# Kernel optimization log

Measured on AMD Instinct MI355X. Metric: run time of the kernel, lower is better.

The kernel has to match this reference:

```python
import jax, jax.numpy as jnp
import numpy as np

MARGIN = 1.0
EPS = 1e-12


def setup_inputs() -> dict:
    key = jax.random.key(0)
    k1, k2, k3 = jax.random.split(key, 3)
    inputs = jax.random.normal(k1, (8192, 128), dtype=jnp.float32)
    targets = jax.random.randint(k2, (8192,), 0, 64, dtype=jnp.int64)
    center = jax.random.normal(k3, (16, 128), dtype=jnp.float32)
    return {"inputs": inputs, "targets": targets, "center": center}


def reference(inputs, targets, center):
    n = inputs.shape[0]
    # pairwise Euclidean distances via ||a||^2 + ||b||^2 - 2 a.b  (matches addmm_ trick)
    sq = jnp.sum(inputs * inputs, axis=1)                      # [n]
    dist2 = sq[:, None] + sq[None, :] - 2.0 * (inputs @ inputs.T)
    dist = jnp.sqrt(jnp.clip(dist2, EPS))                      # [n, n]

    mask = targets[:, None] == targets[None, :]                # same-class mask [n, n]

    # batch-hard mining, fully vectorized (replaces per-row python loops)
    dist_ap = jnp.max(jnp.where(mask, dist, -jnp.inf), axis=1)  # hardest positive
    neg_min = jnp.min(jnp.where(mask, jnp.inf, dist), axis=1)   # hardest negative
    has_neg = jnp.any(~mask, axis=1)
    dist_an = jnp.where(has_neg, neg_min, dist_ap + MARGIN)

    # center augmentation: min over distances to L2-normalized prototypes
    cn = center / jnp.linalg.norm(center, axis=1, keepdims=True)       # [P, d]
    dc = jnp.sqrt(jnp.sum((inputs[:, None, :] - cn[None, :, :]) ** 2, axis=-1))  # [n, P]
    dc = jnp.clip(dc, EPS)
    dist_an = jnp.minimum(dist_an, jnp.min(dc, axis=1))

    # MarginRankingLoss with y=1: mean(relu(dist_ap - dist_an + margin))
    loss = jnp.mean(jnp.maximum(dist_ap - dist_an + MARGIN, 0.0))
    return loss
```

## Files before the change

kernel.cpp:

```cpp
#include <hip/hip_runtime.h>


#define N_ROWS 8192
#define DIM 128
#define KDIM 192
#define ROWB 384
#define NPROTO 16
#define MARGIN_F 1.0f
#define EPS_F 1e-12f
#define BIAS_F 32768.0f

typedef __attribute__((ext_vector_type(8))) short short8;
typedef __attribute__((ext_vector_type(4))) float float4v;
typedef __attribute__((ext_vector_type(4))) unsigned uint4v;

static __device__ __forceinline__ unsigned f2bf(float f) {
  unsigned u = __float_as_uint(f);
  u += 0x7fffu + ((u >> 16) & 1u);
  return u >> 16;
}

static __device__ __forceinline__ void gload_lds16(const void* g, void* l) {
  __builtin_amdgcn_global_load_lds(
      (const __attribute__((address_space(1))) unsigned*)g,
      (__attribute__((address_space(3))) unsigned*)l, 16, 0, 0);
}

__global__ void prep_kernel(const float* __restrict__ x,
                            const float* __restrict__ center,
                            const int* __restrict__ tgt,
                            char* __restrict__ xbf,
                            float* __restrict__ sq,
                            float* __restrict__ mindc,
                            float* __restrict__ out) {
  __shared__ float scn[NPROTO * DIM];
  int tid = threadIdx.x;
  if (blockIdx.x == 0 && tid == 0) out[0] = 0.0f;
  int rloc = tid >> 4, l = tid & 15;
  {
    float v[8];
    float ss = 0.f;
#pragma unroll
    for (int j = 0; j < 8; ++j) {
      v[j] = center[rloc * DIM + l * 8 + j];
      ss += v[j] * v[j];
    }
#pragma unroll
    for (int m = 1; m < 16; m <<= 1) ss += __shfl_xor(ss, m, 64);
    float inv = 1.0f / sqrtf(ss);
#pragma unroll
    for (int j = 0; j < 8; ++j) scn[rloc * DIM + l * 8 + j] = v[j] * inv;
  }
  __syncthreads();

  int row = blockIdx.x * 16 + rloc;
  float4 v0 = ((const float4*)x)[row * 32 + l * 2];
  float4 v1 = ((const float4*)x)[row * 32 + l * 2 + 1];
  float ss = v0.x * v0.x + v0.y * v0.y + v0.z * v0.z + v0.w * v0.w +
             v1.x * v1.x + v1.y * v1.y + v1.z * v1.z + v1.w * v1.w;
  float dots[NPROTO];
#pragma unroll
  for (int p = 0; p < NPROTO; ++p) {
    const float* c = &scn[p * DIM + l * 8];
    dots[p] = v0.x * c[0] + v0.y * c[1] + v0.z * c[2] + v0.w * c[3] +
              v1.x * c[4] + v1.y * c[5] + v1.z * c[6] + v1.w * c[7];
  }
#pragma unroll
  for (int m = 1; m < 16; m <<= 1) {
    ss += __shfl_xor(ss, m, 64);
#pragma unroll
    for (int p = 0; p < NPROTO; ++p) dots[p] += __shfl_xor(dots[p], m, 64);
  }
  uint4 pk;
  pk.x = f2bf(v0.x) | (f2bf(v0.y) << 16);
  pk.y = f2bf(v0.z) | (f2bf(v0.w) << 16);
  pk.z = f2bf(v1.x) | (f2bf(v1.y) << 16);
  pk.w = f2bf(v1.z) | (f2bf(v1.w) << 16);
  *(uint4*)(xbf + (size_t)row * ROWB + l * 16) = pk;
  int cls = tgt[row];
  if (l < 8) {
    unsigned wv = (cls & 1) ? 0xC3000000u : 0x0000C300u;
    uint4 oh;
    oh.x = ((cls >> 1) == (l * 4 + 0)) ? wv : 0u;
    oh.y = ((cls >> 1) == (l * 4 + 1)) ? wv : 0u;
    oh.z = ((cls >> 1) == (l * 4 + 2)) ? wv : 0u;
    oh.w = ((cls >> 1) == (l * 4 + 3)) ? wv : 0u;
    *(uint4*)(xbf + (size_t)row * ROWB + 256 + l * 16) = oh;
  }
  if (l == 0) {
    float mind2 = INFINITY;
#pragma unroll
    for (int p = 0; p < NPROTO; ++p)
      mind2 = fminf(mind2, ss + 1.0f - 2.0f * dots[p]);
    sq[row] = ss;
    mindc[row] = fmaxf(sqrtf(fmaxf(mind2, 0.0f)), EPS_F);
  }
}

__global__ __launch_bounds__(256, 2) void
pairdist_kernel(const char* __restrict__ xbf, const float* __restrict__ sq,
                float* __restrict__ pmax, float* __restrict__ pmin) {
  __shared__ __align__(16) char bl[2][24576];
  const int bid = blockIdx.x;
  const int rg = bid >> 4;
  const int strip = bid & 15;
  const int wave = threadIdx.x >> 6, lane = threadIdx.x & 63;
  const int q = lane >> 4, l16 = lane & 15;
  const int rowbase = rg * 256 + wave * 64;
  const int stripbase = strip * 512;

  const int slot = wave * 64 + lane;
  const char* const srcstrip = xbf + (size_t)stripbase * ROWB;
  int soff[6];
#pragma unroll
  for (int r = 0; r < 6; ++r) {
    int o = r * 4096 + slot * 16;
    int c = o / ROWB;
    soff[r] = c * ROWB + ((o - c * ROWB) ^ ((c & 7) << 4));
  }

  auto stage = [&](int s, char* buf) {
    const char* g = srcstrip + (size_t)s * 24576;
#pragma unroll
    for (int r = 0; r < 6; ++r)
      gload_lds16(g + soff[r], buf + r * 4096 + wave * 1024);
  };

  stage(0, bl[0]);

  short8 a[4][6];
#pragma unroll
  for (int rt = 0; rt < 4; ++rt) {
    const char* ar = xbf + (size_t)(rowbase + rt * 16 + l16) * ROWB + q * 16;
#pragma unroll
    for (int kc = 0; kc < 6; ++kc) a[rt][kc] = *(const short8*)(ar + kc * 64);
#pragma unroll
    for (int kc = 4; kc < 6; ++kc) {
      uint4v u = __builtin_bit_cast(uint4v, a[rt][kc]);
      u ^= 0x80008000u;
      a[rt][kc] = __builtin_bit_cast(short8, u);
    }
  }

  int roffb[6];
#pragma unroll
  for (int kc = 0; kc < 6; ++kc)
    roffb[kc] = (l16 * ROWB + kc * 64 + q * 16) ^ ((l16 & 7) << 4);

  float maxp[16], minn[16];
#pragma unroll
  for (int i = 0; i < 16; ++i) {
    maxp[i] = -INFINITY;
    minn[i] = INFINITY;
  }

#pragma unroll 1
  for (int s = 0; s < 8; ++s) {
    __syncthreads();
    if (s + 1 < 8) stage(s + 1, bl[(s + 1) & 1]);
    const char* cur = bl[s & 1];
    float sqs[4];
#pragma unroll
    for (int ss = 0; ss < 4; ++ss)
      sqs[ss] = sq[stripbase + s * 64 + ss * 16 + l16];
#pragma unroll
    for (int ss = 0; ss < 4; ++ss) {
      const char* bufp = cur + ss * 6144;
      short8 b[6];
#pragma unroll
      for (int kc = 0; kc < 6; ++kc)
        b[kc] = *(const short8*)(bufp + roffb[kc]);
      float4v acc[4];
#pragma unroll
      for (int rt = 0; rt < 4; ++rt) acc[rt] = (float4v){0.f, 0.f, 0.f, 0.f};
#pragma unroll
      for (int kc = 0; kc < 6; ++kc)
#pragma unroll
        for (int rt = 0; rt < 4; ++rt)
          acc[rt] = __builtin_amdgcn_mfma_f32_16x16x32_bf16(a[rt][kc], b[kc],
                                                            acc[rt], 0, 0, 0);
#pragma unroll
      for (int rt = 0; rt < 4; ++rt)
#pragma unroll
        for (int r = 0; r < 4; ++r) {
          float v = fmaf(-2.0f, acc[rt][r], sqs[ss]);
          int idx = rt * 4 + r;
          maxp[idx] = fmaxf(maxp[idx], v);
          minn[idx] = fminf(minn[idx], v);
        }
    }
  }

#pragma unroll
  for (int m = 1; m < 16; m <<= 1)
#pragma unroll
    for (int i = 0; i < 16; ++i) {
      maxp[i] = fmaxf(maxp[i], __shfl_xor(maxp[i], m, 64));
      minn[i] = fminf(minn[i], __shfl_xor(minn[i], m, 64));
    }
  if (l16 == 0) {
    float* pM = pmax + (size_t)strip * N_ROWS + rowbase + q * 4;
    float* pm = pmin + (size_t)strip * N_ROWS + rowbase + q * 4;
#pragma unroll
    for (int rt = 0; rt < 4; ++rt)
#pragma unroll
      for (int r = 0; r < 4; ++r) {
        pM[rt * 16 + r] = maxp[rt * 4 + r];
        pm[rt * 16 + r] = minn[rt * 4 + r];
      }
  }
}

__global__ void finalize_kernel(const float* __restrict__ pmax,
                                const float* __restrict__ pmin,
                                const float* __restrict__ sq,
                                const float* __restrict__ mindc,
                                float* __restrict__ out) {
  __shared__ float wsum[4];
  int i = blockIdx.x * 256 + threadIdx.x;
  float maxv = -INFINITY, minv = INFINITY;
#pragma unroll
  for (int s = 0; s < 16; ++s) {
    maxv = fmaxf(maxv, pmax[s * N_ROWS + i]);
    minv = fminf(minv, pmin[s * N_ROWS + i]);
  }
  float si = sq[i];
  float dap = sqrtf(fmaxf(si + (maxv - BIAS_F), EPS_F));
  float dan = (minv > 16384.0f) ? (dap + MARGIN_F)
                                : sqrtf(fmaxf(si + minv, EPS_F));
  dan = fminf(dan, mindc[i]);
  float c = fmaxf(dap - dan + MARGIN_F, 0.0f) * (1.0f / (float)N_ROWS);
#pragma unroll
  for (int m = 1; m < 64; m <<= 1) c += __shfl_xor(c, m, 64);
  int lane = threadIdx.x & 63, wv = threadIdx.x >> 6;
  if (lane == 0) wsum[wv] = c;
  __syncthreads();
  if (threadIdx.x == 0) atomicAdd(out, wsum[0] + wsum[1] + wsum[2] + wsum[3]);
}

extern "C" void kernel_launch(void* const* d_in, const int* in_sizes, int n_in,
                              void* d_out, int out_size, void* d_ws, size_t ws_size,
                              hipStream_t stream) {
  const float* inputs = (const float*)d_in[0];
  const int* targets = (const int*)d_in[1];
  const float* center = (const float*)d_in[2];
  char* ws = (char*)d_ws;
  char* xbf    = ws;
  float* sq    = (float*)(ws + 3145728);
  float* mindc = (float*)(ws + 3178496);
  float* pmax  = (float*)(ws + 3211264);
  float* pmin  = (float*)(ws + 3735552);
  float* out   = (float*)d_out;

  prep_kernel<<<512, 256, 0, stream>>>(inputs, center, targets, xbf, sq, mindc, out);
  pairdist_kernel<<<512, 256, 0, stream>>>(xbf, sq, pmax, pmin);
  finalize_kernel<<<32, 256, 0, stream>>>(pmax, pmin, sq, mindc, out);
}
```

Measured before the change: 92.99 us.

## Exploit distance-matrix symmetry by computing only upper-triangular 256x256 tiles

The pairwise kernel now launches 528 blocks covering only the upper-triangular 256x256 tiles (I<=J) instead of 512 blocks covering the full matrix. Each off-diagonal tile also derives column-wise max/min by reducing across lanes and waves through shared memory, then writes those as partials for the transposed rows. This roughly halves MFMA work, at the cost of an extra column reduction, shared-memory traffic, a second partial buffer layout (32 strips) and a longer finalize loop. Each block does half the columns it did before, so fixed per-block overhead weighs more.

```diff
diff --git a/kernel.cpp b/kernel.cpp
--- a/kernel.cpp
+++ b/kernel.cpp
@@ -6,6 +6,7 @@
 #define KDIM 192
 #define ROWB 384
 #define NPROTO 16
+#define NRG 32
 #define MARGIN_F 1.0f
 #define EPS_F 1e-12f
 #define BIAS_F 32768.0f
@@ -101,16 +102,17 @@
 pairdist_kernel(const char* __restrict__ xbf, const float* __restrict__ sq,
                 float* __restrict__ pmax, float* __restrict__ pmin) {
   __shared__ __align__(16) char bl[2][24576];
-  const int bid = blockIdx.x;
-  const int rg = bid >> 4;
-  const int strip = bid & 15;
+  __shared__ float cmaxw[4][256], cminw[4][256];
+  int t = blockIdx.x, I = 0;
+  while (t >= NRG - I) { t -= NRG - I; ++I; }
+  const int J = I + t;
   const int wave = threadIdx.x >> 6, lane = threadIdx.x & 63;
   const int q = lane >> 4, l16 = lane & 15;
-  const int rowbase = rg * 256 + wave * 64;
-  const int stripbase = strip * 512;
+  const int rowbase = I * 256 + wave * 64;
+  const int colbase = J * 256;
 
   const int slot = wave * 64 + lane;
-  const char* const srcstrip = xbf + (size_t)stripbase * ROWB;
+  const char* const srcstrip = xbf + (size_t)colbase * ROWB;
   int soff[6];
 #pragma unroll
   for (int r = 0; r < 6; ++r) {
@@ -141,6 +143,12 @@
       a[rt][kc] = __builtin_bit_cast(short8, u);
     }
   }
+  float sqr[16];
+#pragma unroll
+  for (int rt = 0; rt < 4; ++rt)
+#pragma unroll
+    for (int r = 0; r < 4; ++r)
+      sqr[rt * 4 + r] = sq[rowbase + rt * 16 + q * 4 + r];
 
   int roffb[6];
 #pragma unroll
@@ -155,14 +163,15 @@
   }
 
 #pragma unroll 1
-  for (int s = 0; s < 8; ++s) {
+  for (int s = 0; s < 4; ++s) {
     __syncthreads();
-    if (s + 1 < 8) stage(s + 1, bl[(s + 1) & 1]);
+    if (s + 1 < 4) stage(s + 1, bl[(s + 1) & 1]);
     const char* cur = bl[s & 1];
     float sqs[4];
 #pragma unroll
     for (int ss = 0; ss < 4; ++ss)
-      sqs[ss] = sq[stripbase + s * 64 + ss * 16 + l16];
+      sqs[ss] = sq[colbase + s * 64 + ss * 16 + l16];
+    float cmx[4], cmn[4];
 #pragma unroll
     for (int ss = 0; ss < 4; ++ss) {
       const char* bufp = cur + ss * 6144;
@@ -188,6 +197,32 @@
           maxp[idx] = fmaxf(maxp[idx], v);
           minn[idx] = fminf(minn[idx], v);
         }
+      if (I != J) {
+        float um = -INFINITY, un = INFINITY;
+#pragma unroll
+        for (int rt = 0; rt < 4; ++rt)
+#pragma unroll
+          for (int r = 0; r < 4; ++r) {
+            float u = fmaf(-2.0f, acc[rt][r], sqr[rt * 4 + r]);
+            um = fmaxf(um, u);
+            un = fminf(un, u);
+          }
+        cmx[ss] = um;
+        cmn[ss] = un;
+      }
+    }
+    if (I != J) {
+#pragma unroll
+      for (int ss = 0; ss < 4; ++ss) {
+        float a1 = fmaxf(cmx[ss], __shfl_xor(cmx[ss], 16, 64));
+        a1 = fmaxf(a1, __shfl_xor(a1, 32, 64));
+        float a2 = fminf(cmn[ss], __shfl_xor(cmn[ss], 16, 64));
+        a2 = fminf(a2, __shfl_xor(a2, 32, 64));
+        if (q == 0) {
+          cmaxw[wave][s * 64 + ss * 16 + l16] = a1;
+          cminw[wave][s * 64 + ss * 16 + l16] = a2;
+        }
+      }
     }
   }
 
@@ -199,8 +234,8 @@
       minn[i] = fminf(minn[i], __shfl_xor(minn[i], m, 64));
     }
   if (l16 == 0) {
-    float* pM = pmax + (size_t)strip * N_ROWS + rowbase + q * 4;
-    float* pm = pmin + (size_t)strip * N_ROWS + rowbase + q * 4;
+    float* pM = pmax + (size_t)J * N_ROWS + rowbase + q * 4;
+    float* pm = pmin + (size_t)J * N_ROWS + rowbase + q * 4;
 #pragma unroll
     for (int rt = 0; rt < 4; ++rt)
 #pragma unroll
@@ -208,6 +243,16 @@
         pM[rt * 16 + r] = maxp[rt * 4 + r];
         pm[rt * 16 + r] = minn[rt * 4 + r];
       }
+  }
+  if (I != J) {
+    __syncthreads();
+    int c = threadIdx.x;
+    float M = fmaxf(fmaxf(cmaxw[0][c], cmaxw[1][c]),
+                    fmaxf(cmaxw[2][c], cmaxw[3][c]));
+    float m = fminf(fminf(cminw[0][c], cminw[1][c]),
+                    fminf(cminw[2][c], cminw[3][c]));
+    pmax[(size_t)I * N_ROWS + colbase + c] = M;
+    pmin[(size_t)I * N_ROWS + colbase + c] = m;
   }
 }
 
@@ -220,7 +265,7 @@
   int i = blockIdx.x * 256 + threadIdx.x;
   float maxv = -INFINITY, minv = INFINITY;
 #pragma unroll
-  for (int s = 0; s < 16; ++s) {
+  for (int s = 0; s < NRG; ++s) {
     maxv = fmaxf(maxv, pmax[s * N_ROWS + i]);
     minv = fminf(minv, pmin[s * N_ROWS + i]);
   }
@@ -249,10 +294,10 @@
   float* sq    = (float*)(ws + 3145728);
   float* mindc = (float*)(ws + 3178496);
   float* pmax  = (float*)(ws + 3211264);
-  float* pmin  = (float*)(ws + 3735552);
+  float* pmin  = (float*)(ws + 4259840);
   float* out   = (float*)d_out;
 
   prep_kernel<<<512, 256, 0, stream>>>(inputs, center, targets, xbf, sq, mindc, out);
-  pairdist_kernel<<<512, 256, 0, stream>>>(xbf, sq, pmax, pmin);
+  pairdist_kernel<<<528, 256, 0, stream>>>(xbf, sq, pmax, pmin);
   finalize_kernel<<<32, 256, 0, stream>>>(pmax, pmin, sq, mindc, out);
 }
```

Result: slower. 110.7 us (+19.0%).

## Give each wave a private triple-buffered LDS pipeline to remove block barriers

Applied to the files above, without the earlier changes.

Each wave now streams its own 16-row chunks of the column strip into a private three-deep LDS ring, using explicit vmcnt waits instead of block-wide __syncthreads. MFMA sections are also wrapped in s_setprio to favour matrix issue. This removes barrier stalls between waves and deepens prefetch. In exchange, every wave loads the whole B strip itself, roughly quadrupling L2-to-LDS traffic and raising LDS use per block. The hand-written waitcnt counts also rely on how the compiler orders the per-chunk sq loads.

```diff
diff --git a/kernel.cpp b/kernel.cpp
--- a/kernel.cpp
+++ b/kernel.cpp
@@ -6,6 +6,8 @@
 #define KDIM 192
 #define ROWB 384
 #define NPROTO 16
+#define NSTRIP 16
+#define NCHUNK 32
 #define MARGIN_F 1.0f
 #define EPS_F 1e-12f
 #define BIAS_F 32768.0f
@@ -100,33 +102,29 @@
 __global__ __launch_bounds__(256, 2) void
 pairdist_kernel(const char* __restrict__ xbf, const float* __restrict__ sq,
                 float* __restrict__ pmax, float* __restrict__ pmin) {
-  __shared__ __align__(16) char bl[2][24576];
-  const int bid = blockIdx.x;
-  const int rg = bid >> 4;
-  const int strip = bid & 15;
+  __shared__ __align__(16) char bl[4][3 * 6144];
   const int wave = threadIdx.x >> 6, lane = threadIdx.x & 63;
   const int q = lane >> 4, l16 = lane & 15;
+  const int rg = blockIdx.x >> 4, strip = blockIdx.x & 15;
   const int rowbase = rg * 256 + wave * 64;
   const int stripbase = strip * 512;
-
-  const int slot = wave * 64 + lane;
-  const char* const srcstrip = xbf + (size_t)stripbase * ROWB;
+  char* const mybuf = bl[wave];
+
   int soff[6];
 #pragma unroll
   for (int r = 0; r < 6; ++r) {
-    int o = r * 4096 + slot * 16;
+    int o = r * 1024 + lane * 16;
     int c = o / ROWB;
     soff[r] = c * ROWB + ((o - c * ROWB) ^ ((c & 7) << 4));
   }
-
-  auto stage = [&](int s, char* buf) {
-    const char* g = srcstrip + (size_t)s * 24576;
-#pragma unroll
-    for (int r = 0; r < 6; ++r)
-      gload_lds16(g + soff[r], buf + r * 4096 + wave * 1024);
+  const char* const srcstrip = xbf + (size_t)stripbase * ROWB;
+
+  auto stage = [&](int ch, int bi) {
+    const char* g = srcstrip + (size_t)ch * 6144;
+    char* d = mybuf + bi * 6144;
+#pragma unroll
+    for (int r = 0; r < 6; ++r) gload_lds16(g + soff[r], d + r * 1024);
   };
-
-  stage(0, bl[0]);
 
   short8 a[4][6];
 #pragma unroll
@@ -141,6 +139,16 @@
       a[rt][kc] = __builtin_bit_cast(short8, u);
     }
   }
+#pragma unroll
+  for (int rt = 0; rt < 4; ++rt)
+#pragma unroll
+    for (int kc = 0; kc < 6; ++kc)
+      asm volatile("" : "+v"(a[rt][kc]));
+
+  asm volatile("s_waitcnt vmcnt(0)" ::: "memory");
+  stage(0, 0);
+  stage(1, 1);
+  stage(2, 2);
 
   int roffb[6];
 #pragma unroll
@@ -149,46 +157,45 @@
 
   float maxp[16], minn[16];
 #pragma unroll
-  for (int i = 0; i < 16; ++i) {
-    maxp[i] = -INFINITY;
-    minn[i] = INFINITY;
-  }
-
+  for (int i = 0; i < 16; ++i) { maxp[i] = -INFINITY; minn[i] = INFINITY; }
+
+  int bi = 0;
 #pragma unroll 1
-  for (int s = 0; s < 8; ++s) {
-    __syncthreads();
-    if (s + 1 < 8) stage(s + 1, bl[(s + 1) & 1]);
-    const char* cur = bl[s & 1];
-    float sqs[4];
-#pragma unroll
-    for (int ss = 0; ss < 4; ++ss)
-      sqs[ss] = sq[stripbase + s * 64 + ss * 16 + l16];
-#pragma unroll
-    for (int ss = 0; ss < 4; ++ss) {
-      const char* bufp = cur + ss * 6144;
-      short8 b[6];
-#pragma unroll
-      for (int kc = 0; kc < 6; ++kc)
-        b[kc] = *(const short8*)(bufp + roffb[kc]);
-      float4v acc[4];
-#pragma unroll
-      for (int rt = 0; rt < 4; ++rt) acc[rt] = (float4v){0.f, 0.f, 0.f, 0.f};
-#pragma unroll
-      for (int kc = 0; kc < 6; ++kc)
-#pragma unroll
-        for (int rt = 0; rt < 4; ++rt)
-          acc[rt] = __builtin_amdgcn_mfma_f32_16x16x32_bf16(a[rt][kc], b[kc],
-                                                            acc[rt], 0, 0, 0);
+  for (int c = 0; c < NCHUNK; ++c) {
+    if (c < NCHUNK - 2)
+      asm volatile("s_waitcnt vmcnt(12)" ::: "memory");
+    else if (c == NCHUNK - 2)
+      asm volatile("s_waitcnt vmcnt(6)" ::: "memory");
+    else
+      asm volatile("s_waitcnt vmcnt(0)" ::: "memory");
+    float sqc = sq[stripbase + c * 16 + l16];
+    const char* bufp = mybuf + bi * 6144;
+    short8 b[6];
+#pragma unroll
+    for (int kc = 0; kc < 6; ++kc) b[kc] = *(const short8*)(bufp + roffb[kc]);
+    asm volatile("s_waitcnt lgkmcnt(0)" ::: "memory");
+    if (c + 3 < NCHUNK) stage(c + 3, bi);
+    float4v acc[4];
+#pragma unroll
+    for (int rt = 0; rt < 4; ++rt) acc[rt] = (float4v){0.f, 0.f, 0.f, 0.f};
+    __builtin_amdgcn_s_setprio(1);
+#pragma unroll
+    for (int kc = 0; kc < 6; ++kc)
 #pragma unroll
       for (int rt = 0; rt < 4; ++rt)
-#pragma unroll
-        for (int r = 0; r < 4; ++r) {
-          float v = fmaf(-2.0f, acc[rt][r], sqs[ss]);
-          int idx = rt * 4 + r;
-          maxp[idx] = fmaxf(maxp[idx], v);
-          minn[idx] = fminf(minn[idx], v);
-        }
-    }
+        acc[rt] = __builtin_amdgcn_mfma_f32_16x16x32_bf16(a[rt][kc], b[kc],
+                                                          acc[rt], 0, 0, 0);
+    __builtin_amdgcn_s_setprio(0);
+#pragma unroll
+    for (int rt = 0; rt < 4; ++rt)
+#pragma unroll
+      for (int r = 0; r < 4; ++r) {
+        float v = fmaf(-2.0f, acc[rt][r], sqc);
+        int idx = rt * 4 + r;
+        maxp[idx] = fmaxf(maxp[idx], v);
+        minn[idx] = fminf(minn[idx], v);
+      }
+    if (++bi == 3) bi = 0;
   }
 
 #pragma unroll
@@ -220,7 +227,7 @@
   int i = blockIdx.x * 256 + threadIdx.x;
   float maxv = -INFINITY, minv = INFINITY;
 #pragma unroll
-  for (int s = 0; s < 16; ++s) {
+  for (int s = 0; s < NSTRIP; ++s) {
     maxv = fmaxf(maxv, pmax[s * N_ROWS + i]);
     minv = fminf(minv, pmin[s * N_ROWS + i]);
   }
```

Measured after the change: 98.28 us. +5.7%, slower.

## Switch pairwise-distance GEMM to 32x32x16 bf16 MFMA tiles

Applied to the files above, without the earlier changes.

Replaces the 16x16x32 MFMA tiling with 32x32x16 MFMA, so each wave computes two 32-row tiles against 32-column slices. Each B fragment read from LDS now feeds two MFMAs, and the register layout and final row/column reduction are rewritten to match the 32x32 output layout. Raises s_setprio around the MFMA loop and relaxes launch bounds to one block per SIMD pair, trading occupancy for more registers (32 max/min accumulators plus 16-wide accumulators).

```diff
diff --git a/kernel.cpp b/kernel.cpp
--- a/kernel.cpp
+++ b/kernel.cpp
@@ -6,12 +6,13 @@
 #define KDIM 192
 #define ROWB 384
 #define NPROTO 16
+#define NSTRIP 16
 #define MARGIN_F 1.0f
 #define EPS_F 1e-12f
 #define BIAS_F 32768.0f
 
 typedef __attribute__((ext_vector_type(8))) short short8;
-typedef __attribute__((ext_vector_type(4))) float float4v;
+typedef __attribute__((ext_vector_type(16))) float f32x16;
 typedef __attribute__((ext_vector_type(4))) unsigned uint4v;
 
 static __device__ __forceinline__ unsigned f2bf(float f) {
@@ -97,19 +98,17 @@
   }
 }
 
-__global__ __launch_bounds__(256, 2) void
+__global__ __launch_bounds__(256, 1) void
 pairdist_kernel(const char* __restrict__ xbf, const float* __restrict__ sq,
                 float* __restrict__ pmax, float* __restrict__ pmin) {
   __shared__ __align__(16) char bl[2][24576];
-  const int bid = blockIdx.x;
-  const int rg = bid >> 4;
-  const int strip = bid & 15;
   const int wave = threadIdx.x >> 6, lane = threadIdx.x & 63;
-  const int q = lane >> 4, l16 = lane & 15;
+  const int c31 = lane & 31, h = lane >> 5;
+  const int rg = blockIdx.x >> 4, strip = blockIdx.x & 15;
   const int rowbase = rg * 256 + wave * 64;
   const int stripbase = strip * 512;
 
-  const int slot = wave * 64 + lane;
+  const int slot = threadIdx.x;
   const char* const srcstrip = xbf + (size_t)stripbase * ROWB;
   int soff[6];
 #pragma unroll
@@ -128,85 +127,87 @@
 
   stage(0, bl[0]);
 
-  short8 a[4][6];
-#pragma unroll
-  for (int rt = 0; rt < 4; ++rt) {
-    const char* ar = xbf + (size_t)(rowbase + rt * 16 + l16) * ROWB + q * 16;
-#pragma unroll
-    for (int kc = 0; kc < 6; ++kc) a[rt][kc] = *(const short8*)(ar + kc * 64);
-#pragma unroll
-    for (int kc = 4; kc < 6; ++kc) {
-      uint4v u = __builtin_bit_cast(uint4v, a[rt][kc]);
+  short8 a[2][12];
+#pragma unroll
+  for (int t = 0; t < 2; ++t) {
+    const char* ar =
+        xbf + (size_t)(rowbase + t * 32 + c31) * ROWB + h * 16;
+#pragma unroll
+    for (int kc = 0; kc < 12; ++kc) a[t][kc] = *(const short8*)(ar + kc * 32);
+#pragma unroll
+    for (int kc = 8; kc < 12; ++kc) {
+      uint4v u = __builtin_bit_cast(uint4v, a[t][kc]);
       u ^= 0x80008000u;
-      a[rt][kc] = __builtin_bit_cast(short8, u);
-    }
-  }
-
-  int roffb[6];
-#pragma unroll
-  for (int kc = 0; kc < 6; ++kc)
-    roffb[kc] = (l16 * ROWB + kc * 64 + q * 16) ^ ((l16 & 7) << 4);
-
-  float maxp[16], minn[16];
-#pragma unroll
-  for (int i = 0; i < 16; ++i) {
-    maxp[i] = -INFINITY;
-    minn[i] = INFINITY;
-  }
+      a[t][kc] = __builtin_bit_cast(short8, u);
+    }
+  }
+#pragma unroll
+  for (int t = 0; t < 2; ++t)
+#pragma unroll
+    for (int kc = 0; kc < 12; ++kc)
+      asm volatile("" : "+v"(a[t][kc]));
+
+  int roff[12];
+#pragma unroll
+  for (int kc = 0; kc < 12; ++kc)
+    roff[kc] = (c31 * ROWB + kc * 32 + h * 16) ^ ((c31 & 7) << 4);
+
+  float maxp[32], minn[32];
+#pragma unroll
+  for (int i = 0; i < 32; ++i) { maxp[i] = -INFINITY; minn[i] = INFINITY; }
 
 #pragma unroll 1
   for (int s = 0; s < 8; ++s) {
     __syncthreads();
     if (s + 1 < 8) stage(s + 1, bl[(s + 1) & 1]);
     const char* cur = bl[s & 1];
-    float sqs[4];
-#pragma unroll
-    for (int ss = 0; ss < 4; ++ss)
-      sqs[ss] = sq[stripbase + s * 64 + ss * 16 + l16];
-#pragma unroll
-    for (int ss = 0; ss < 4; ++ss) {
-      const char* bufp = cur + ss * 6144;
-      short8 b[6];
-#pragma unroll
-      for (int kc = 0; kc < 6; ++kc)
-        b[kc] = *(const short8*)(bufp + roffb[kc]);
-      float4v acc[4];
-#pragma unroll
-      for (int rt = 0; rt < 4; ++rt) acc[rt] = (float4v){0.f, 0.f, 0.f, 0.f};
-#pragma unroll
-      for (int kc = 0; kc < 6; ++kc)
-#pragma unroll
-        for (int rt = 0; rt < 4; ++rt)
-          acc[rt] = __builtin_amdgcn_mfma_f32_16x16x32_bf16(a[rt][kc], b[kc],
-                                                            acc[rt], 0, 0, 0);
-#pragma unroll
-      for (int rt = 0; rt < 4; ++rt)
-#pragma unroll
-        for (int r = 0; r < 4; ++r) {
-          float v = fmaf(-2.0f, acc[rt][r], sqs[ss]);
-          int idx = rt * 4 + r;
-          maxp[idx] = fmaxf(maxp[idx], v);
-          minn[idx] = fminf(minn[idx], v);
-        }
-    }
-  }
-
-#pragma unroll
-  for (int m = 1; m < 16; m <<= 1)
-#pragma unroll
-    for (int i = 0; i < 16; ++i) {
+    float sqs[2];
+    sqs[0] = sq[stripbase + s * 64 + c31];
+    sqs[1] = sq[stripbase + s * 64 + 32 + c31];
+#pragma unroll
+    for (int c2 = 0; c2 < 2; ++c2) {
+      const char* bufp = cur + c2 * 12288;
+      f32x16 acc0 = {}, acc1 = {};
+      __builtin_amdgcn_s_setprio(1);
+#pragma unroll
+      for (int kc = 0; kc < 12; ++kc) {
+        short8 b = *(const short8*)(bufp + roff[kc]);
+        acc0 = __builtin_amdgcn_mfma_f32_32x32x16_bf16(a[0][kc], b, acc0,
+                                                       0, 0, 0);
+        acc1 = __builtin_amdgcn_mfma_f32_32x32x16_bf16(a[1][kc], b, acc1,
+                                                       0, 0, 0);
+      }
+      __builtin_amdgcn_s_setprio(0);
+      float sqc = sqs[c2];
+#pragma unroll
+      for (int r = 0; r < 16; ++r) {
+        float v0 = fmaf(-2.0f, acc0[r], sqc);
+        float v1 = fmaf(-2.0f, acc1[r], sqc);
+        maxp[r] = fmaxf(maxp[r], v0);
+        minn[r] = fminf(minn[r], v0);
+        maxp[16 + r] = fmaxf(maxp[16 + r], v1);
+        minn[16 + r] = fminf(minn[16 + r], v1);
+      }
+    }
+  }
+
+#pragma unroll
+  for (int m = 1; m < 32; m <<= 1)
+#pragma unroll
+    for (int i = 0; i < 32; ++i) {
       maxp[i] = fmaxf(maxp[i], __shfl_xor(maxp[i], m, 64));
       minn[i] = fminf(minn[i], __shfl_xor(minn[i], m, 64));
     }
-  if (l16 == 0) {
-    float* pM = pmax + (size_t)strip * N_ROWS + rowbase + q * 4;
-    float* pm = pmin + (size_t)strip * N_ROWS + rowbase + q * 4;
-#pragma unroll
-    for (int rt = 0; rt < 4; ++rt)
-#pragma unroll
-      for (int r = 0; r < 4; ++r) {
-        pM[rt * 16 + r] = maxp[rt * 4 + r];
-        pm[rt * 16 + r] = minn[rt * 4 + r];
+  if (c31 == 0) {
+    float* pM = pmax + (size_t)strip * N_ROWS + rowbase;
+    float* pm = pmin + (size_t)strip * N_ROWS + rowbase;
+#pragma unroll
+    for (int t = 0; t < 2; ++t)
+#pragma unroll
+      for (int r = 0; r < 16; ++r) {
+        int rowl = t * 32 + (r & 3) + 8 * (r >> 2) + 4 * h;
+        pM[rowl] = maxp[t * 16 + r];
+        pm[rowl] = minn[t * 16 + r];
       }
   }
 }
@@ -220,7 +221,7 @@
   int i = blockIdx.x * 256 + threadIdx.x;
   float maxv = -INFINITY, minv = INFINITY;
 #pragma unroll
-  for (int s = 0; s < 16; ++s) {
+  for (int s = 0; s < NSTRIP; ++s) {
     maxv = fmaxf(maxv, pmax[s * N_ROWS + i]);
     minv = fminf(minv, pmin[s * N_ROWS + i]);
   }
```

Result: slower. 111.6 us (+20.0%).
